# Optimization experiments

Measured on AMD Instinct MI355X. Metric: run time of the kernel, lower is better.

The kernel has to match this reference:

```python
import jax, jax.numpy as jnp
import numpy as np

N, K, F, E = 50000, 32, 128, 8

def setup_inputs() -> dict:
    key = jax.random.key(0)
    k1, k2, k3, k4, k5 = jax.random.split(key, 5)
    nodes = jax.random.normal(k1, (N, F), dtype=jnp.float32)
    nlist = jax.random.randint(k2, (N, K), 0, N, dtype=jnp.int64)
    edges = jax.random.normal(k3, (N, K, E), dtype=jnp.float32)
    inv_degree = jax.random.uniform(k4, (N,), dtype=jnp.float32)
    w = jax.random.normal(k5, (F, F, E), dtype=jnp.float32)
    return {"nodes": nodes, "nlist": nlist, "edges": edges,
            "inv_degree": inv_degree, "w": w}

def reference(nodes, nlist, edges, inv_degree, w):
    # gather neighbor features: [N, K, F]
    sliced = nodes[nlist]
    # 3-way contraction with neighbor-sum and inverse-degree scaling
    # edges: ijn (N,K,E); sliced: ijl (N,K,F); w: lmn (F,F,E); inv_degree: i
    out = jnp.einsum('ijn,ijl,lmn,i->im', edges, sliced, w, inv_degree)
    # activation is None (linear) per init_kwargs
    return out
```

## Files before the change

### kernel.cpp

```cpp
#include <hip/hip_runtime.h>
#include <hip/hip_bf16.h>

static constexpr int NN  = 50000;
static constexpr int KNB = 32;
static constexpr int F   = 128;
static constexpr int E   = 8;
static constexpr int TI  = 16;
static constexpr int LN  = F * E;

typedef __attribute__((ext_vector_type(8))) short short8v;
typedef __attribute__((ext_vector_type(4))) float f32x4;

__device__ __forceinline__ unsigned short f2bf(float x) {
    unsigned u = __float_as_uint(x);
    unsigned r = (u + 0x7fff + ((u >> 16) & 1)) >> 16;
    return (unsigned short)r;
}
__device__ __forceinline__ float bf2f_lo(unsigned g) { return __uint_as_float(g << 16); }
__device__ __forceinline__ float bf2f_hi(unsigned g) { return __uint_as_float(g & 0xffff0000u); }

__global__ void prep_w_kernel(const float* __restrict__ w, unsigned short* __restrict__ w2f) {
    int o  = blockIdx.x * 256 + threadIdx.x;
    int e8 = o & 7, kq = (o >> 3) & 3, m = (o >> 5) & 127, kb = o >> 12;
    int k  = kb * 32 + kq * 4 + (e8 & 3) + ((e8 >> 2) << 4);
    int l  = k >> 3, n = k & 7;
    w2f[o] = f2bf(w[(size_t)(l * F + m) * E + n]);
}

__global__ void prep_nodes_kernel(const float* __restrict__ nodes, unsigned short* __restrict__ nb) {
    int t = blockIdx.x * 256 + threadIdx.x;
    const float4* s = (const float4*)nodes + (size_t)t * 2;
    float4 a = s[0], b = s[1];
    uint4 pk;
    pk.x = (unsigned)f2bf(a.x) | ((unsigned)f2bf(a.y) << 16);
    pk.y = (unsigned)f2bf(a.z) | ((unsigned)f2bf(a.w) << 16);
    pk.z = (unsigned)f2bf(b.x) | ((unsigned)f2bf(b.y) << 16);
    pk.w = (unsigned)f2bf(b.z) | ((unsigned)f2bf(b.w) << 16);
    ((uint4*)nb)[t] = pk;
}

#define ISSUE8(GB)                                                         \
    asm volatile(                                                          \
        "global_load_dword %0, %8, %16\n\t"                                \
        "global_load_dword %1, %9, %16\n\t"                                \
        "global_load_dword %2, %10, %16\n\t"                               \
        "global_load_dword %3, %11, %16\n\t"                               \
        "global_load_dword %4, %12, %16\n\t"                               \
        "global_load_dword %5, %13, %16\n\t"                               \
        "global_load_dword %6, %14, %16\n\t"                               \
        "global_load_dword %7, %15, %16"                                   \
        : "=&v"(g[(GB)+0]), "=&v"(g[(GB)+1]), "=&v"(g[(GB)+2]), "=&v"(g[(GB)+3]), \
          "=&v"(g[(GB)+4]), "=&v"(g[(GB)+5]), "=&v"(g[(GB)+6]), "=&v"(g[(GB)+7])  \
        : "v"(vo[0]), "v"(vo[1]), "v"(vo[2]), "v"(vo[3]),                  \
          "v"(vo[4]), "v"(vo[5]), "v"(vo[6]), "v"(vo[7]),                  \
          "s"(nodesBf)                                                     \
        : "memory")

#define MKVO(JB)                                                           \
    _Pragma("unroll")                                                      \
    for (int q = 0; q < 8; ++q) {                                          \
        unsigned idx = (unsigned)nl[(JB) + q];      \
        if (idx >= (unsigned)NN) idx = 0u;                                 \
        vo[q] = idx * 256u + lane4;                                        \
    }

#define WAIT8(NSTR, GB)                                                    \
    asm volatile("s_waitcnt vmcnt(" NSTR ")"                               \
        : "+v"(g[(GB)+0]), "+v"(g[(GB)+1]), "+v"(g[(GB)+2]), "+v"(g[(GB)+3]),  \
          "+v"(g[(GB)+4]), "+v"(g[(GB)+5]), "+v"(g[(GB)+6]), "+v"(g[(GB)+7])   \
        :: "memory")

#define CONSUME8(JB, GB)                                                   \
    _Pragma("unroll")                                                      \
    for (int q = 0; q < 8; ++q) {                                          \
        const int j = (JB) + q;                                            \
        const float v0 = bf2f_lo(g[(GB) + q]);                             \
        const float v1 = bf2f_hi(g[(GB) + q]);                             \
        const float4 e0 = *(const float4*)(ep + j * 8);       \
        const float4 e1 = *(const float4*)(ep + j * 8 + 4);                \
        a0[0] = __builtin_fmaf(e0.x, v0, a0[0]); a1[0] = __builtin_fmaf(e0.x, v1, a1[0]); \
        a0[1] = __builtin_fmaf(e0.y, v0, a0[1]); a1[1] = __builtin_fmaf(e0.y, v1, a1[1]); \
        a0[2] = __builtin_fmaf(e0.z, v0, a0[2]); a1[2] = __builtin_fmaf(e0.z, v1, a1[2]); \
        a0[3] = __builtin_fmaf(e0.w, v0, a0[3]); a1[3] = __builtin_fmaf(e0.w, v1, a1[3]); \
        a0[4] = __builtin_fmaf(e1.x, v0, a0[4]); a1[4] = __builtin_fmaf(e1.x, v1, a1[4]); \
        a0[5] = __builtin_fmaf(e1.y, v0, a0[5]); a1[5] = __builtin_fmaf(e1.y, v1, a1[5]); \
        a0[6] = __builtin_fmaf(e1.z, v0, a0[6]); a1[6] = __builtin_fmaf(e1.z, v1, a1[6]); \
        a0[7] = __builtin_fmaf(e1.w, v0, a0[7]); a1[7] = __builtin_fmaf(e1.w, v1, a1[7]); \
    }

__global__ __launch_bounds__(512, 8)
void mp_main_kernel(const unsigned short* __restrict__ nodesBf,
                    const int*   __restrict__ nlist,
                    const float* __restrict__ edges,
                    const float* __restrict__ inv_degree,
                    const unsigned short* __restrict__ w2f,
                    float* __restrict__ out)
{
    __shared__ unsigned short tS[TI * LN];
    const int tid    = threadIdx.x;
    const int wv     = __builtin_amdgcn_readfirstlane(tid >> 6);
    const int lane   = tid & 63;
    const int i_base = blockIdx.x * TI;
    char* tB = (char*)tS;
    const unsigned lane4 = (unsigned)lane * 4u;

    for (int it = 0; it < 2; ++it) {
        const int row = wv * 2 + it;
        const int i   = i_base + row;
        const int*   nl = nlist + (size_t)i * KNB;
        const float* ep = edges + (size_t)i * (KNB * E);

        float a0[E], a1[E];
        #pragma unroll
        for (int n = 0; n < E; ++n) { a0[n] = 0.f; a1[n] = 0.f; }

        unsigned g[16];
        unsigned vo[8];
        MKVO(0);  ISSUE8(0);
        MKVO(8);  ISSUE8(8);
        WAIT8("8", 0);  CONSUME8(0, 0);
        MKVO(16); ISSUE8(0);
        WAIT8("8", 8);  CONSUME8(8, 8);
        MKVO(24); ISSUE8(8);
        WAIT8("8", 0);  CONSUME8(16, 0);
        WAIT8("0", 8);  CONSUME8(24, 8);

        uint4 pk0, pk1;
        asm("v_cvt_pk_bf16_f32 %0, %1, %2" : "=v"(pk0.x) : "v"(a0[0]), "v"(a0[1]));
        asm("v_cvt_pk_bf16_f32 %0, %1, %2" : "=v"(pk0.y) : "v"(a0[2]), "v"(a0[3]));
        asm("v_cvt_pk_bf16_f32 %0, %1, %2" : "=v"(pk0.z) : "v"(a0[4]), "v"(a0[5]));
        asm("v_cvt_pk_bf16_f32 %0, %1, %2" : "=v"(pk0.w) : "v"(a0[6]), "v"(a0[7]));
        asm("v_cvt_pk_bf16_f32 %0, %1, %2" : "=v"(pk1.x) : "v"(a1[0]), "v"(a1[1]));
        asm("v_cvt_pk_bf16_f32 %0, %1, %2" : "=v"(pk1.y) : "v"(a1[2]), "v"(a1[3]));
        asm("v_cvt_pk_bf16_f32 %0, %1, %2" : "=v"(pk1.z) : "v"(a1[4]), "v"(a1[5]));
        asm("v_cvt_pk_bf16_f32 %0, %1, %2" : "=v"(pk1.w) : "v"(a1[6]), "v"(a1[7]));
        const int p2 = (lane >> 2) & 1;
        const int s  = (row & 7) << 4;
        const int rb = row * (LN * 2);
        const uint4 first  = p2 ? pk1 : pk0;
        const uint4 second = p2 ? pk0 : pk1;
        *(uint4*)(tB + rb + ((lane * 32 + (p2 << 4))      ^ s)) = first;
        *(uint4*)(tB + rb + ((lane * 32 + 16 - (p2 << 4)) ^ s)) = second;
    }
    __syncthreads();

    const int colm = lane & 15;
    const int kq   = lane >> 4;
    const int mt   = wv;

    f32x4 c0 = {0.f, 0.f, 0.f, 0.f};

    const int arow = colm * (LN * 2);
    const int asw  = (colm & 7) << 4;

    #pragma unroll 4
    for (int kb = 0; kb < LN / 32; ++kb) {
        union { short8v v; uint2 u[2]; } af;
        af.u[0] = *(const uint2*)(tB + arow + ((kb * 64      + kq * 8) ^ asw));
        af.u[1] = *(const uint2*)(tB + arow + ((kb * 64 + 32 + kq * 8) ^ asw));
        union { short8v v; uint4 u; } b0;
        b0.u = *(const uint4*)(w2f + ((size_t)((kb * 128 + mt * 16 + colm) * 4 + kq)) * 8);
        c0 = __builtin_amdgcn_mfma_f32_16x16x32_bf16(af.v, b0.v, c0, 0, 0, 0);
    }

    #pragma unroll
    for (int r = 0; r < 4; ++r) {
        const int ii = kq * 4 + r;
        const int gi = i_base + ii;
        out[(size_t)gi * F + mt * 16 + colm] = inv_degree[gi] * c0[r];
    }
}

__global__ __launch_bounds__(256, 2)
void mp_fused_fallback(const float* __restrict__ nodes, const int* __restrict__ nlist,
                       const float* __restrict__ edges, const float* __restrict__ inv_degree,
                       const float* __restrict__ w, float* __restrict__ out)
{
    __shared__ float tLds[TI * F * E];
    const int tid = threadIdx.x;
    const int i_base = blockIdx.x * TI;
    {
        const int l = tid & (F - 1);
        const int half = __builtin_amdgcn_readfirstlane(tid >> 7);
        for (int g = 0; g < TI / 2; ++g) {
            const int ii = g * 2 + half;
            const int i = i_base + ii;
            float acc[E];
            #pragma unroll
            for (int n = 0; n < E; ++n) acc[n] = 0.f;
            const int* nl = nlist + i * KNB;
            const float* ep = edges + (size_t)i * (KNB * E);
            #pragma unroll 4
            for (int j = 0; j < KNB; ++j) {
                unsigned idx = (unsigned)nl[j];
                if (idx >= (unsigned)NN) idx = 0u;
                const float v = nodes[idx * F + l];
                #pragma unroll
                for (int n = 0; n < E; ++n) acc[n] = __builtin_fmaf(ep[j * E + n], v, acc[n]);
            }
            float4* dst = (float4*)&tLds[ii * (F * E) + l * E];
            dst[0] = make_float4(acc[0], acc[1], acc[2], acc[3]);
            dst[1] = make_float4(acc[4], acc[5], acc[6], acc[7]);
        }
    }
    __syncthreads();
    const int m_lo = tid & 63;
    const int q = __builtin_amdgcn_readfirstlane(tid >> 6);
    float accA[TI], accB[TI];
    #pragma unroll
    for (int ii = 0; ii < TI; ++ii) { accA[ii] = 0.f; accB[ii] = 0.f; }
    for (int lq = 0; lq < F / 4; ++lq) {
        const int l = q * (F / 4) + lq;
        const float4* wp0 = (const float4*)&w[(size_t)l * (F * E) + (size_t)m_lo * E];
        const float4* wp1 = (const float4*)&w[(size_t)l * (F * E) + (size_t)(m_lo + 64) * E];
        const float4 w0a = wp0[0], w0b = wp0[1];
        const float4 w1a = wp1[0], w1b = wp1[1];
        #pragma unroll
        for (int ii = 0; ii < TI; ++ii) {
            const float4* tp = (const float4*)&tLds[ii * (F * E) + l * E];
            const float4 ta = tp[0], tb = tp[1];
            float sA = accA[ii], sB = accB[ii];
            sA = __builtin_fmaf(ta.x, w0a.x, sA); sA = __builtin_fmaf(ta.y, w0a.y, sA);
            sA = __builtin_fmaf(ta.z, w0a.z, sA); sA = __builtin_fmaf(ta.w, w0a.w, sA);
            sA = __builtin_fmaf(tb.x, w0b.x, sA); sA = __builtin_fmaf(tb.y, w0b.y, sA);
            sA = __builtin_fmaf(tb.z, w0b.z, sA); sA = __builtin_fmaf(tb.w, w0b.w, sA);
            sB = __builtin_fmaf(ta.x, w1a.x, sB); sB = __builtin_fmaf(ta.y, w1a.y, sB);
            sB = __builtin_fmaf(ta.z, w1a.z, sB); sB = __builtin_fmaf(ta.w, w1a.w, sB);
            sB = __builtin_fmaf(tb.x, w1b.x, sB); sB = __builtin_fmaf(tb.y, w1b.y, sB);
            sB = __builtin_fmaf(tb.z, w1b.z, sB); sB = __builtin_fmaf(tb.w, w1b.w, sB);
            accA[ii] = sA; accB[ii] = sB;
        }
    }
    __syncthreads();
    float* pLds = tLds;
    #pragma unroll
    for (int ii = 0; ii < TI; ++ii) {
        pLds[q * (TI * F) + ii * F + m_lo] = accA[ii];
        pLds[q * (TI * F) + ii * F + m_lo + 64] = accB[ii];
    }
    __syncthreads();
    #pragma unroll
    for (int r = 0; r < (TI * F) / 256; ++r) {
        const int o = r * 256 + tid;
        const int ii = o >> 7;
        const int m = o & (F - 1);
        const float s = pLds[0 * (TI * F) + ii * F + m] + pLds[1 * (TI * F) + ii * F + m]
                      + pLds[2 * (TI * F) + ii * F + m] + pLds[3 * (TI * F) + ii * F + m];
        const int i = i_base + ii;
        out[(size_t)i * F + m] = inv_degree[i] * s;
    }
}

extern "C" void kernel_launch(void* const* d_in, const int* in_sizes, int n_in,
                              void* d_out, int out_size, void* d_ws, size_t ws_size,
                              hipStream_t stream) {
    const float* nodes      = (const float*)d_in[0];
    const int*   nlist      = (const int*)d_in[1];
    const float* edges      = (const float*)d_in[2];
    const float* inv_degree = (const float*)d_in[3];
    const float* w          = (const float*)d_in[4];
    float* out = (float*)d_out;
    (void)in_sizes; (void)n_in; (void)out_size;

    const size_t need_w2 = (size_t)LN * F * 2;
    const size_t need_nb = (size_t)NN * F * 2;

    if (ws_size < need_w2 + need_nb) {
        mp_fused_fallback<<<dim3(NN / TI), dim3(256), 0, stream>>>(
            nodes, nlist, edges, inv_degree, w, out);
        return;
    }
    unsigned short* w2f = (unsigned short*)d_ws;
    unsigned short* nb  = (unsigned short*)((char*)d_ws + need_w2);

    prep_w_kernel<<<dim3((LN * F) / 256), dim3(256), 0, stream>>>(w, w2f);
    prep_nodes_kernel<<<dim3(NN * F / 8 / 256), dim3(256), 0, stream>>>(nodes, nb);
    mp_main_kernel<<<dim3(NN / TI), dim3(512), 0, stream>>>(
        nb, nlist, edges, inv_degree, w2f, out);
}
```

Baseline: 94.30 us.

## Pipeline neighbor gathers across both rows with triple-buffered loads

Replaces the per-row loop with one software pipeline spanning both rows a wave handles. It keeps three batches of eight gathered loads in flight instead of two, so the second row's loads issue while the first row is still being consumed and stored. It also removes the out-of-range index clamp and the memory clobbers on the inline-asm loads and waits. This gives the compiler more freedom but risks reordering around the asm and faulting on bad indices, and it uses more registers for the larger load buffer.

```diff
diff --git a/kernel.cpp b/kernel.cpp
--- a/kernel.cpp
+++ b/kernel.cpp
@@ -39,7 +39,7 @@
     ((uint4*)nb)[t] = pk;
 }
 
-#define ISSUE8(GB)                                                         \
+#define ISSUE8(GS)                                                         \
     asm volatile(                                                          \
         "global_load_dword %0, %8, %16\n\t"                                \
         "global_load_dword %1, %9, %16\n\t"                                \
@@ -49,35 +49,30 @@
         "global_load_dword %5, %13, %16\n\t"                               \
         "global_load_dword %6, %14, %16\n\t"                               \
         "global_load_dword %7, %15, %16"                                   \
-        : "=&v"(g[(GB)+0]), "=&v"(g[(GB)+1]), "=&v"(g[(GB)+2]), "=&v"(g[(GB)+3]), \
-          "=&v"(g[(GB)+4]), "=&v"(g[(GB)+5]), "=&v"(g[(GB)+6]), "=&v"(g[(GB)+7])  \
+        : "=&v"(g[(GS)+0]), "=&v"(g[(GS)+1]), "=&v"(g[(GS)+2]), "=&v"(g[(GS)+3]), \
+          "=&v"(g[(GS)+4]), "=&v"(g[(GS)+5]), "=&v"(g[(GS)+6]), "=&v"(g[(GS)+7])  \
         : "v"(vo[0]), "v"(vo[1]), "v"(vo[2]), "v"(vo[3]),                  \
           "v"(vo[4]), "v"(vo[5]), "v"(vo[6]), "v"(vo[7]),                  \
-          "s"(nodesBf)                                                     \
-        : "memory")
-
-#define MKVO(JB)                                                           \
+          "s"(nodesBf))
+
+#define MKVO(NLP, JB)                                                      \
     _Pragma("unroll")                                                      \
-    for (int q = 0; q < 8; ++q) {                                          \
-        unsigned idx = (unsigned)nl[(JB) + q];      \
-        if (idx >= (unsigned)NN) idx = 0u;                                 \
-        vo[q] = idx * 256u + lane4;                                        \
-    }
-
-#define WAIT8(NSTR, GB)                                                    \
+    for (int q = 0; q < 8; ++q)                                            \
+        vo[q] = (unsigned)(NLP)[(JB) + q] * 256u + lane4;
+
+#define WAIT8(NSTR, GS)                                                    \
     asm volatile("s_waitcnt vmcnt(" NSTR ")"                               \
-        : "+v"(g[(GB)+0]), "+v"(g[(GB)+1]), "+v"(g[(GB)+2]), "+v"(g[(GB)+3]),  \
-          "+v"(g[(GB)+4]), "+v"(g[(GB)+5]), "+v"(g[(GB)+6]), "+v"(g[(GB)+7])   \
-        :: "memory")
-
-#define CONSUME8(JB, GB)                                                   \
+        : "+v"(g[(GS)+0]), "+v"(g[(GS)+1]), "+v"(g[(GS)+2]), "+v"(g[(GS)+3]),  \
+          "+v"(g[(GS)+4]), "+v"(g[(GS)+5]), "+v"(g[(GS)+6]), "+v"(g[(GS)+7]))
+
+#define CONSUME8(EPP, JB, GS)                                              \
     _Pragma("unroll")                                                      \
     for (int q = 0; q < 8; ++q) {                                          \
         const int j = (JB) + q;                                            \
-        const float v0 = bf2f_lo(g[(GB) + q]);                             \
-        const float v1 = bf2f_hi(g[(GB) + q]);                             \
-        const float4 e0 = *(const float4*)(ep + j * 8);       \
-        const float4 e1 = *(const float4*)(ep + j * 8 + 4);                \
+        const float v0 = bf2f_lo(g[(GS) + q]);                             \
+        const float v1 = bf2f_hi(g[(GS) + q]);                             \
+        const float4 e0 = *(const float4*)((EPP) + j * 8);    \
+        const float4 e1 = *(const float4*)((EPP) + j * 8 + 4);             \
         a0[0] = __builtin_fmaf(e0.x, v0, a0[0]); a1[0] = __builtin_fmaf(e0.x, v1, a1[0]); \
         a0[1] = __builtin_fmaf(e0.y, v0, a0[1]); a1[1] = __builtin_fmaf(e0.y, v1, a1[1]); \
         a0[2] = __builtin_fmaf(e0.z, v0, a0[2]); a1[2] = __builtin_fmaf(e0.z, v1, a1[2]); \
@@ -86,6 +81,28 @@
         a0[5] = __builtin_fmaf(e1.y, v0, a0[5]); a1[5] = __builtin_fmaf(e1.y, v1, a1[5]); \
         a0[6] = __builtin_fmaf(e1.z, v0, a0[6]); a1[6] = __builtin_fmaf(e1.z, v1, a1[6]); \
         a0[7] = __builtin_fmaf(e1.w, v0, a0[7]); a1[7] = __builtin_fmaf(e1.w, v1, a1[7]); \
+    }
+
+#define STORE_ROW(ROW)                                                     \
+    {                                                                      \
+        uint4 pk0, pk1;                                                    \
+        asm("v_cvt_pk_bf16_f32 %0, %1, %2" : "=v"(pk0.x) : "v"(a0[0]), "v"(a0[1])); \
+        asm("v_cvt_pk_bf16_f32 %0, %1, %2" : "=v"(pk0.y) : "v"(a0[2]), "v"(a0[3])); \
+        asm("v_cvt_pk_bf16_f32 %0, %1, %2" : "=v"(pk0.z) : "v"(a0[4]), "v"(a0[5])); \
+        asm("v_cvt_pk_bf16_f32 %0, %1, %2" : "=v"(pk0.w) : "v"(a0[6]), "v"(a0[7])); \
+        asm("v_cvt_pk_bf16_f32 %0, %1, %2" : "=v"(pk1.x) : "v"(a1[0]), "v"(a1[1])); \
+        asm("v_cvt_pk_bf16_f32 %0, %1, %2" : "=v"(pk1.y) : "v"(a1[2]), "v"(a1[3])); \
+        asm("v_cvt_pk_bf16_f32 %0, %1, %2" : "=v"(pk1.z) : "v"(a1[4]), "v"(a1[5])); \
+        asm("v_cvt_pk_bf16_f32 %0, %1, %2" : "=v"(pk1.w) : "v"(a1[6]), "v"(a1[7])); \
+        const int p2 = (lane >> 2) & 1;                                    \
+        const int s  = ((ROW) & 7) << 4;                                   \
+        const int rb = (ROW) * (LN * 2);                                   \
+        const uint4 first  = p2 ? pk1 : pk0;                               \
+        const uint4 second = p2 ? pk0 : pk1;                               \
+        *(uint4*)(tB + rb + ((lane * 32 + (p2 << 4))      ^ s)) = first;   \
+        *(uint4*)(tB + rb + ((lane * 32 + 16 - (p2 << 4)) ^ s)) = second;  \
+        _Pragma("unroll")                                                  \
+        for (int n = 0; n < E; ++n) { a0[n] = 0.f; a1[n] = 0.f; }          \
     }
 
 __global__ __launch_bounds__(512, 8)
@@ -104,43 +121,32 @@
     char* tB = (char*)tS;
     const unsigned lane4 = (unsigned)lane * 4u;
 
-    for (int it = 0; it < 2; ++it) {
-        const int row = wv * 2 + it;
-        const int i   = i_base + row;
-        const int*   nl = nlist + (size_t)i * KNB;
-        const float* ep = edges + (size_t)i * (KNB * E);
+    {
+        const int i0 = i_base + wv * 2;
+        const int*   nl0 = nlist + (size_t)i0 * KNB;
+        const int*   nl1 = nl0 + KNB;
+        const float* ep0 = edges + (size_t)i0 * (KNB * E);
+        const float* ep1 = ep0 + KNB * E;
+        const int row0 = wv * 2, row1 = wv * 2 + 1;
 
         float a0[E], a1[E];
         #pragma unroll
         for (int n = 0; n < E; ++n) { a0[n] = 0.f; a1[n] = 0.f; }
 
-        unsigned g[16];
+        unsigned g[24];
         unsigned vo[8];
-        MKVO(0);  ISSUE8(0);
-        MKVO(8);  ISSUE8(8);
-        WAIT8("8", 0);  CONSUME8(0, 0);
-        MKVO(16); ISSUE8(0);
-        WAIT8("8", 8);  CONSUME8(8, 8);
-        MKVO(24); ISSUE8(8);
-        WAIT8("8", 0);  CONSUME8(16, 0);
-        WAIT8("0", 8);  CONSUME8(24, 8);
-
-        uint4 pk0, pk1;
-        asm("v_cvt_pk_bf16_f32 %0, %1, %2" : "=v"(pk0.x) : "v"(a0[0]), "v"(a0[1]));
-        asm("v_cvt_pk_bf16_f32 %0, %1, %2" : "=v"(pk0.y) : "v"(a0[2]), "v"(a0[3]));
-        asm("v_cvt_pk_bf16_f32 %0, %1, %2" : "=v"(pk0.z) : "v"(a0[4]), "v"(a0[5]));
-        asm("v_cvt_pk_bf16_f32 %0, %1, %2" : "=v"(pk0.w) : "v"(a0[6]), "v"(a0[7]));
-        asm("v_cvt_pk_bf16_f32 %0, %1, %2" : "=v"(pk1.x) : "v"(a1[0]), "v"(a1[1]));
-        asm("v_cvt_pk_bf16_f32 %0, %1, %2" : "=v"(pk1.y) : "v"(a1[2]), "v"(a1[3]));
-        asm("v_cvt_pk_bf16_f32 %0, %1, %2" : "=v"(pk1.z) : "v"(a1[4]), "v"(a1[5]));
-        asm("v_cvt_pk_bf16_f32 %0, %1, %2" : "=v"(pk1.w) : "v"(a1[6]), "v"(a1[7]));
-        const int p2 = (lane >> 2) & 1;
-        const int s  = (row & 7) << 4;
-        const int rb = row * (LN * 2);
-        const uint4 first  = p2 ? pk1 : pk0;
-        const uint4 second = p2 ? pk0 : pk1;
-        *(uint4*)(tB + rb + ((lane * 32 + (p2 << 4))      ^ s)) = first;
-        *(uint4*)(tB + rb + ((lane * 32 + 16 - (p2 << 4)) ^ s)) = second;
+        MKVO(nl0, 0);  ISSUE8(0);
+        MKVO(nl0, 8);  ISSUE8(8);
+        MKVO(nl0, 16); ISSUE8(16);
+        WAIT8("16", 0);  CONSUME8(ep0, 0, 0);   MKVO(nl0, 24); ISSUE8(0);
+        WAIT8("16", 8);  CONSUME8(ep0, 8, 8);   MKVO(nl1, 0);  ISSUE8(8);
+        WAIT8("16", 16); CONSUME8(ep0, 16, 16); MKVO(nl1, 8);  ISSUE8(16);
+        WAIT8("16", 0);  CONSUME8(ep0, 24, 0);  STORE_ROW(row0);
+                                                MKVO(nl1, 16); ISSUE8(0);
+        WAIT8("16", 8);  CONSUME8(ep1, 0, 8);   MKVO(nl1, 24); ISSUE8(8);
+        WAIT8("16", 16); CONSUME8(ep1, 8, 16);
+        WAIT8("8", 0);   CONSUME8(ep1, 16, 0);
+        WAIT8("0", 8);   CONSUME8(ep1, 24, 8);  STORE_ROW(row1);
     }
     __syncthreads();
 
```

New measurement: 96.59 us. +2.4%, slower.
